# Performance work log

Hardware: AMD Instinct MI355X
Metric: run time of the kernel (lower is better)

Reference implementation:

```python
import jax, jax.numpy as jnp
import numpy as np

N_NODES = 100000
N_EDGES = 1600000
NUM_GRAPHS = 1000
NODE_IN, EDGE_IN = 32, 16
NODE_EMB, EDGE_EMB, HID, OUT, L = 64, 32, 64, 1, 3
EPS = 1e-5


def _glorot(key, shape):
    fan_in = shape[0]
    return jax.random.normal(key, shape, jnp.float32) / np.sqrt(fan_in)


def setup_inputs() -> dict:
    key = jax.random.key(0)
    ks = jax.random.split(key, 16)
    inp = {
        "x": jax.random.normal(ks[0], (N_NODES, NODE_IN), jnp.float32),
        "edge_attr": jax.random.normal(ks[1], (N_EDGES, EDGE_IN), jnp.float32),
        "edge_index": jax.random.randint(ks[2], (2, N_EDGES), 0, N_NODES, jnp.int64
                                         if jax.config.jax_enable_x64 else jnp.int32),
        "batch": jnp.sort(jax.random.randint(ks[3], (N_NODES,), 0, NUM_GRAPHS)),
        # embeddings
        "node_W": _glorot(ks[4], (NODE_IN, NODE_EMB)),
        "node_b": jnp.zeros((NODE_EMB,), jnp.float32),
        "edge_W": _glorot(ks[5], (EDGE_IN, EDGE_EMB)),
        "edge_b": jnp.zeros((EDGE_EMB,), jnp.float32),
        # per-layer MPNN params (node_dim==64 for every layer since node_emb_dim==hidden_dim)
        "msg_W": _glorot(ks[6], (L, NODE_EMB + EDGE_EMB, HID)),
        "msg_b": jnp.zeros((L, HID), jnp.float32),
        "msg_gamma": jnp.ones((L, HID), jnp.float32),
        "msg_beta": jnp.zeros((L, HID), jnp.float32),
        "upd_W": _glorot(ks[7], (L, NODE_EMB + HID, HID)),
        "upd_b": jnp.zeros((L, HID), jnp.float32),
        "upd_gamma": jnp.ones((L, HID), jnp.float32),
        "upd_beta": jnp.zeros((L, HID), jnp.float32),
        # readout
        "r1_W": _glorot(ks[8], (HID, HID)),
        "r1_b": jnp.zeros((HID,), jnp.float32),
        "r2_W": _glorot(ks[9], (HID, OUT)),
        "r2_b": jnp.zeros((OUT,), jnp.float32),
    }
    return inp


def _bn(h, gamma, beta):
    # BatchNorm1d in training mode: normalize with batch mean / biased variance
    mu = jnp.mean(h, axis=0)
    var = jnp.mean(jnp.square(h - mu), axis=0)
    return gamma * (h - mu) * jax.lax.rsqrt(var + EPS) + beta


def reference(x, edge_attr, edge_index, batch,
              node_W, node_b, edge_W, edge_b,
              msg_W, msg_b, msg_gamma, msg_beta,
              upd_W, upd_b, upd_gamma, upd_beta,
              r1_W, r1_b, r2_W, r2_b):
    h = x @ node_W + node_b                       # [N, 64]
    e = edge_attr @ edge_W + edge_b               # [E, 32]
    src, dst = edge_index[0], edge_index[1]
    for i in range(L):
        # message: gather x_j, concat edge feats, Linear-ReLU-BN (dropout = eval/no-op)
        m = jnp.concatenate([h[src], e], axis=-1) @ msg_W[i] + msg_b[i]   # [E, 64]
        m = _bn(jax.nn.relu(m), msg_gamma[i], msg_beta[i])
        # aggregate: scatter-add to destination nodes
        agg = jax.ops.segment_sum(m, dst, num_segments=N_NODES)          # [N, 64]
        # update: concat self feats, Linear-ReLU-BN
        u = jnp.concatenate([h, agg], axis=-1) @ upd_W[i] + upd_b[i]     # [N, 64]
        h = _bn(jax.nn.relu(u), upd_gamma[i], upd_beta[i])
    # global add pool over graphs
    g = jax.ops.segment_sum(h, batch, num_segments=NUM_GRAPHS)           # [G, 64]
    out = jax.nn.relu(g @ r1_W + r1_b) @ r2_W + r2_b                     # [G, 1]
    return out
```

## Files before the change

kernel.cpp:

```cpp
#include <hip/hip_runtime.h>
#include <hip/hip_bf16.h>

#define N_NODES   100000
#define N_EDGES   1600000
#define NUM_GRAPHS 1000

typedef unsigned int u32;
typedef unsigned short u16;

typedef __bf16 bf16_t;
typedef bf16_t bf16x8 __attribute__((ext_vector_type(8)));
typedef float  f32x4  __attribute__((ext_vector_type(4)));

__device__ __forceinline__ float bf2f(u16 u){ return __uint_as_float(((u32)u)<<16); }
__device__ __forceinline__ float BL(u32 u){ return __uint_as_float(u<<16); }
__device__ __forceinline__ float BH(u32 u){ return __uint_as_float(u&0xffff0000u); }
__device__ __forceinline__ u16 f2bf(float f){
  u32 u = __float_as_uint(f);
  return (u16)((u + 0x7fffu + ((u>>16)&1u)) >> 16);
}
__device__ __forceinline__ float ldf(const void* p, size_t i, int isbf){
  return isbf ? bf2f(((const u16*)p)[i]) : ((const float*)p)[i];
}

union U4BF { uint4 u; bf16x8 v; };

__global__ void k_detect(const u32* __restrict__ x, int* __restrict__ flag){
  int t = threadIdx.x; int cnt = 0;
  for (int i = t; i < 256; i += 64){
    u32 w = x[i];
    u32 e = (w >> 7) & 0xffu;
    if (e >= 110u && e <= 137u) cnt++;
  }
  for (int o = 32; o; o >>= 1) cnt += __shfl_xor(cnt, o);
  if (t == 0) *flag = (cnt > 128) ? 1 : 0;
}

__global__ void k_prep(const void* __restrict__ eW, const void* __restrict__ eb,
                       const void* __restrict__ mW, const void* __restrict__ mb,
                       u16* __restrict__ Weff, const int* __restrict__ flagp){
  int isbf = *flagp;
  int l = blockIdx.x, c = threadIdx.x;
  u16* W = Weff + ((size_t)l*64 + c)*96;
  for (int k = 0; k < 64; k++)
    W[k] = f2bf(ldf(mW, (size_t)(l*96 + k)*64 + c, isbf));
  for (int j = 0; j < 16; j++){
    float acc = 0.f;
    for (int k = 0; k < 32; k++)
      acc += ldf(eW, (size_t)j*32 + k, isbf) * ldf(mW, (size_t)(l*96 + 64 + k)*64 + c, isbf);
    W[64 + j] = f2bf(acc);
  }
  float fbv = ldf(mb, (size_t)l*64 + c, isbf);
  for (int k = 0; k < 32; k++)
    fbv += ldf(eb, k, isbf) * ldf(mW, (size_t)(l*96 + 64 + k)*64 + c, isbf);
  W[80] = f2bf(fbv);
  for (int k = 81; k < 96; k++) W[k] = 0;
}

__global__ void k_updprep(const void* __restrict__ uW, const void* __restrict__ ub,
                          const float* __restrict__ maff,
                          u16* __restrict__ Wupd, float* __restrict__ biasv,
                          float* __restrict__ tvv, const int* __restrict__ flagp, int l){
  int isbf = *flagp; int c = threadIdx.x;
  u16* W = Wupd + (size_t)c*192;
  float tv = 0.f;
  for (int k = 0; k < 64; k++){
    float wka = ldf(uW, (size_t)(l*128 + k)*64 + c, isbf);
    W[k] = f2bf(wka);
    float wkb = ldf(uW, (size_t)(l*128 + 64 + k)*64 + c, isbf);
    float prod = wkb * maff[k];
    u16 hi = f2bf(prod);
    W[64 + k]  = hi;
    W[128 + k] = f2bf(prod - bf2f(hi));
    tv = fmaf(maff[64 + k], wkb, tv);
  }
  biasv[c] = ldf(ub, (size_t)l*64 + c, isbf);
  tvv[c] = tv;
}

__global__ void k_node_emb(const void* __restrict__ x, const void* __restrict__ nW,
                           const void* __restrict__ nb, u16* __restrict__ hsp,
                           const int* __restrict__ flagp){
  int isbf = *flagp;
  int lane = threadIdx.x & 63;
  int gw = (blockIdx.x*blockDim.x + threadIdx.x) >> 6;
  int nw = (gridDim.x*blockDim.x) >> 6;
  float w[32];
#pragma unroll
  for (int k = 0; k < 32; k++) w[k] = ldf(nW, (size_t)k*64 + lane, isbf);
  float bias = ldf(nb, lane, isbf);
  for (int n = gw; n < N_NODES; n += nw){
    float acc = bias;
    if (isbf){
      const uint4* xr = (const uint4*)((const u16*)x + (size_t)n*32);
#pragma unroll
      for (int q = 0; q < 4; q++){
        uint4 a = xr[q];
        u32 uu[4] = {a.x, a.y, a.z, a.w};
#pragma unroll
        for (int j = 0; j < 4; j++){
          acc = fmaf(BL(uu[j]), w[q*8 + 2*j + 0], acc);
          acc = fmaf(BH(uu[j]), w[q*8 + 2*j + 1], acc);
        }
      }
    } else {
      const float4* xr = (const float4*)((const float*)x + (size_t)n*32);
#pragma unroll
      for (int q = 0; q < 8; q++){
        float4 a = xr[q];
        acc = fmaf(a.x, w[q*4+0], acc); acc = fmaf(a.y, w[q*4+1], acc);
        acc = fmaf(a.z, w[q*4+2], acc); acc = fmaf(a.w, w[q*4+3], acc);
      }
    }
    u16 hi = f2bf(acc);
    hsp[(size_t)n*128 + lane]      = hi;
    hsp[(size_t)n*128 + 64 + lane] = f2bf(acc - bf2f(hi));
  }
}

__global__ void k_deg(const int* __restrict__ ei, int* __restrict__ deg){
  int i = blockIdx.x*blockDim.x + threadIdx.x;
  int stride = gridDim.x*blockDim.x;
  for (int e = i; e < N_EDGES; e += stride)
    atomicAdd(&deg[ei[N_EDGES + e]], 1);
}

__global__ void __launch_bounds__(256) k_scan1(const int* __restrict__ deg,
                                               int* __restrict__ bsum){
  __shared__ int wsum[4];
  int b = blockIdx.x, t = threadIdx.x;
  int i0 = b*512 + t;
  int s = 0;
  if (i0 < N_NODES) s += deg[i0];
  if (i0 + 256 < N_NODES) s += deg[i0 + 256];
  for (int o = 32; o; o >>= 1) s += __shfl_xor(s, o);
  if ((t & 63) == 0) wsum[t >> 6] = s;
  __syncthreads();
  if (t == 0) bsum[b] = wsum[0] + wsum[1] + wsum[2] + wsum[3];
}

__global__ void k_scan2(const int* __restrict__ bsum, int* __restrict__ boff,
                        int* __restrict__ rp){
  __shared__ int l[200];
  int t = threadIdx.x;
  if (t < 196) l[t] = bsum[t];
  __syncthreads();
  if (t == 0){
    int r = 0;
    for (int k = 0; k < 196; k++){ int x = l[k]; l[k] = r; r += x; }
    rp[N_NODES] = r;
  }
  __syncthreads();
  if (t < 196) boff[t] = l[t];
}

__global__ void __launch_bounds__(256) k_scan3(const int* __restrict__ deg,
                        const int* __restrict__ boff, int* __restrict__ rp,
                        int* __restrict__ cursor, float* __restrict__ degf){
  __shared__ int wpre[4];
  int b = blockIdx.x, t = threadIdx.x;
  int i0 = b*512 + 2*t;
  int d0 = (i0     < N_NODES) ? deg[i0]     : 0;
  int d1 = (i0 + 1 < N_NODES) ? deg[i0 + 1] : 0;
  int s = d0 + d1;
  int incl = s;
  for (int o = 1; o < 64; o <<= 1){ int u = __shfl_up(incl, o); if ((t & 63) >= o) incl += u; }
  if ((t & 63) == 63) wpre[t >> 6] = incl;
  __syncthreads();
  if (t == 0){ int r = 0; for (int k = 0; k < 4; k++){ int x = wpre[k]; wpre[k] = r; r += x; } }
  __syncthreads();
  int excl = boff[b] + wpre[t >> 6] + incl - s;
  if (i0 < N_NODES){
    rp[i0] = excl; cursor[i0] = excl; degf[i0] = (float)d0;
  }
  if (i0 + 1 < N_NODES){
    rp[i0+1] = excl + d0; cursor[i0+1] = excl + d0; degf[i0+1] = (float)d1;
  }
}

__global__ void k_scatter(const int* __restrict__ ei, int* __restrict__ cursor,
                          int* __restrict__ perm2){
  int i = blockIdx.x*blockDim.x + threadIdx.x;
  int stride = gridDim.x*blockDim.x;
  for (int e = i; e < N_EDGES; e += stride){
    int d = ei[N_EDGES + e];
    int p = atomicAdd(&cursor[d], 1);
    ((int2*)perm2)[p] = make_int2(ei[e], e);
  }
}

__global__ void k_scatter2(const int* __restrict__ ei, int* __restrict__ cursor,
                           int* __restrict__ perm, u16* __restrict__ eacsr,
                           const void* __restrict__ ea, const int* __restrict__ flagp){
  int isbf = *flagp;
  int i = blockIdx.x*blockDim.x + threadIdx.x;
  int stride = gridDim.x*blockDim.x;
  if (i < 16){
    perm[N_EDGES + i] = 0;
    uint4 z = make_uint4(0,0,0,0);
    uint4* out = (uint4*)(eacsr + (size_t)(N_EDGES + i)*16);
    out[0] = z; out[1] = z;
  }
  for (int e = i; e < N_EDGES; e += stride){
    int d = ei[N_EDGES + e];
    int p = atomicAdd(&cursor[d], 1);
    perm[p] = ei[e];
    uint4 r0, r1;
    if (isbf){
      const uint4* er = (const uint4*)((const u16*)ea + (size_t)e*16);
      r0 = er[0]; r1 = er[1];
    } else {
      const float4* ef = (const float4*)((const float*)ea + (size_t)e*16);
      float4 f0 = ef[0], f1 = ef[1], f2 = ef[2], f3 = ef[3];
      r0.x = (u32)f2bf(f0.x) | ((u32)f2bf(f0.y)<<16);
      r0.y = (u32)f2bf(f0.z) | ((u32)f2bf(f0.w)<<16);
      r0.z = (u32)f2bf(f1.x) | ((u32)f2bf(f1.y)<<16);
      r0.w = (u32)f2bf(f1.z) | ((u32)f2bf(f1.w)<<16);
      r1.x = (u32)f2bf(f2.x) | ((u32)f2bf(f2.y)<<16);
      r1.y = (u32)f2bf(f2.z) | ((u32)f2bf(f2.w)<<16);
      r1.z = (u32)f2bf(f3.x) | ((u32)f2bf(f3.y)<<16);
      r1.w = (u32)f2bf(f3.z) | ((u32)f2bf(f3.w)<<16);
    }
    uint4* out = (uint4*)(eacsr + (size_t)p*16);
    out[0] = r0; out[1] = r1;
  }
}

__device__ __forceinline__ void adv_tile(const int* __restrict__ rp,
                                         int ni, int bi, int ei,
                                         int& no, int& bo, int& eo){
  if (bi + 16 < ei){ no = ni; bo = bi + 16; eo = ei; return; }
  int t = ni + 1;
  int nb = ei;
  int ne = rp[(t < N_NODES) ? t + 1 : N_NODES];
  while (nb == ne && t + 1 < N_NODES){
    t++; nb = ne; ne = rp[t + 1];
  }
  no = t; bo = nb; eo = ne;
}

__global__ void __launch_bounds__(256) k_msgmm(
    const u16* __restrict__ hsp, const void* __restrict__ ea,
    const int* __restrict__ rp, const int* __restrict__ perm2,
    const u16* __restrict__ Weff, u16* __restrict__ aggs,
    float* __restrict__ stats, const int* __restrict__ flagp,
    int l, int nwaves){
  __shared__ float bs[128];
  int tid = threadIdx.x;
  if (tid < 128) bs[tid] = 0.f;
  __syncthreads();
  int isbf = *flagp;
  int lane = tid & 63, wv = tid >> 6;
  int w = blockIdx.x*4 + wv;
  long long t0 = (long long)w     * N_EDGES / nwaves;
  long long t1 = (long long)(w+1) * N_EDGES / nwaves;
  int lo = 0, hi = N_NODES;
  while (lo < hi){ int mid = (lo+hi)>>1; if ((long long)rp[mid] < t0) lo = mid+1; else hi = mid; }
  int n0 = lo, n1;
  if (w == nwaves-1) n1 = N_NODES;
  else {
    lo = 0; hi = N_NODES;
    while (lo < hi){ int mid = (lo+hi)>>1; if ((long long)rp[mid] < t1) lo = mid+1; else hi = mid; }
    n1 = lo;
  }
  int nn = lane & 15, kg = lane >> 4;
  bf16x8 B[3][4];
  const u16* Wl = Weff + (size_t)l*64*96;
#pragma unroll
  for (int t = 0; t < 4; t++)
#pragma unroll
    for (int kb = 0; kb < 3; kb++)
      B[kb][t] = *(const bf16x8*)(Wl + (size_t)(t*16+nn)*96 + kb*32 + kg*8);
  U4BF ac; ac.u = make_uint4((kg==2)? 0x3f80u : 0u, 0u, 0u, 0u);
  float s1[4] = {0,0,0,0}, s2[4] = {0,0,0,0};
  for (int n = n0; n < n1; n++){
    int b0 = rp[n], b1 = rp[n+1];
    float r0 = 0.f, r1 = 0.f, r2 = 0.f, r3 = 0.f;
    for (int base = b0; base < b1; base += 16){
      int rem = b1 - base; if (rem > 16) rem = 16;
      int row = (nn < rem) ? nn : rem-1;
      int2 p = ((const int2*)perm2)[base + row];
      const uint4* hp = (const uint4*)(hsp + (size_t)p.x*128);
      U4BF fA, fB, fC;
      fA.u = hp[kg];
      fB.u = hp[4 + kg];
      if (kg < 2){
        if (isbf){
          fC.u = ((const uint4*)ea)[(size_t)p.y*2 + kg];
        } else {
          const float4* ef = (const float4*)ea;
          float4 f0 = ef[(size_t)p.y*4 + kg*2];
          float4 f1 = ef[(size_t)p.y*4 + kg*2 + 1];
          fC.u.x = (u32)f2bf(f0.x) | ((u32)f2bf(f0.y)<<16);
          fC.u.y = (u32)f2bf(f0.z) | ((u32)f2bf(f0.w)<<16);
          fC.u.z = (u32)f2bf(f1.x) | ((u32)f2bf(f1.y)<<16);
          fC.u.w = (u32)f2bf(f1.z) | ((u32)f2bf(f1.w)<<16);
        }
      } else fC = ac;
      f32x4 a0 = {0,0,0,0}, a1 = {0,0,0,0}, a2 = {0,0,0,0}, a3 = {0,0,0,0};
      a0 = __builtin_amdgcn_mfma_f32_16x16x32_bf16(fA.v, B[0][0], a0, 0,0,0);
      a1 = __builtin_amdgcn_mfma_f32_16x16x32_bf16(fA.v, B[0][1], a1, 0,0,0);
      a2 = __builtin_amdgcn_mfma_f32_16x16x32_bf16(fA.v, B[0][2], a2, 0,0,0);
      a3 = __builtin_amdgcn_mfma_f32_16x16x32_bf16(fA.v, B[0][3], a3, 0,0,0);
      a0 = __builtin_amdgcn_mfma_f32_16x16x32_bf16(fB.v, B[1][0], a0, 0,0,0);
      a1 = __builtin_amdgcn_mfma_f32_16x16x32_bf16(fB.v, B[1][1], a1, 0,0,0);
      a2 = __builtin_amdgcn_mfma_f32_16x16x32_bf16(fB.v, B[1][2], a2, 0,0,0);
      a3 = __builtin_amdgcn_mfma_f32_16x16x32_bf16(fB.v, B[1][3], a3, 0,0,0);
      a0 = __builtin_amdgcn_mfma_f32_16x16x32_bf16(fC.v, B[2][0], a0, 0,0,0);
      a1 = __builtin_amdgcn_mfma_f32_16x16x32_bf16(fC.v, B[2][1], a1, 0,0,0);
      a2 = __builtin_amdgcn_mfma_f32_16x16x32_bf16(fC.v, B[2][2], a2, 0,0,0);
      a3 = __builtin_amdgcn_mfma_f32_16x16x32_bf16(fC.v, B[2][3], a3, 0,0,0);
      int rowbase = kg*4;
      float ts0 = 0.f, ts1 = 0.f, ts2 = 0.f, ts3 = 0.f;
#pragma unroll
      for (int j = 0; j < 4; j++){
        bool valid = (rowbase + j) < rem;
        float m0 = fmaxf(a0[j], 0.f); m0 = valid ? m0 : 0.f;
        float m1 = fmaxf(a1[j], 0.f); m1 = valid ? m1 : 0.f;
        float m2 = fmaxf(a2[j], 0.f); m2 = valid ? m2 : 0.f;
        float m3 = fmaxf(a3[j], 0.f); m3 = valid ? m3 : 0.f;
        ts0 += m0; ts1 += m1; ts2 += m2; ts3 += m3;
        s2[0] = fmaf(m0,m0,s2[0]); s2[1] = fmaf(m1,m1,s2[1]);
        s2[2] = fmaf(m2,m2,s2[2]); s2[3] = fmaf(m3,m3,s2[3]);
      }
      s1[0] += ts0; s1[1] += ts1; s1[2] += ts2; s1[3] += ts3;
      ts0 += __shfl_xor(ts0,16); ts0 += __shfl_xor(ts0,32);
      ts1 += __shfl_xor(ts1,16); ts1 += __shfl_xor(ts1,32);
      ts2 += __shfl_xor(ts2,16); ts2 += __shfl_xor(ts2,32);
      ts3 += __shfl_xor(ts3,16); ts3 += __shfl_xor(ts3,32);
      r0 += ts0; r1 += ts1; r2 += ts2; r3 += ts3;
    }
    float v = (kg==0) ? r0 : (kg==1) ? r1 : (kg==2) ? r2 : r3;
    u16 hiv = f2bf(v);
    aggs[(size_t)n*128 + lane]      = hiv;
    aggs[(size_t)n*128 + 64 + lane] = f2bf(v - bf2f(hiv));
  }
#pragma unroll
  for (int t = 0; t < 4; t++){
    atomicAdd(&bs[t*16+nn], s1[t]);
    atomicAdd(&bs[64+t*16+nn], s2[t]);
  }
  __syncthreads();
  if (tid < 128) atomicAdd(&stats[tid], bs[tid]);
}

__global__ void __launch_bounds__(256) k_msgmm2(
    const u16* __restrict__ hsp, const u16* __restrict__ eacsr,
    const int* __restrict__ rp, const int* __restrict__ perm,
    const u16* __restrict__ Weff, u16* __restrict__ aggs,
    float* __restrict__ stats, int l, int nwaves){
  __shared__ float bs[128];
  int tid = threadIdx.x;
  if (tid < 128) bs[tid] = 0.f;
  __syncthreads();
  int lane = tid & 63;
  int w = blockIdx.x*4 + (tid >> 6);
  long long t0 = (long long)w     * N_EDGES / nwaves;
  long long t1 = (long long)(w+1) * N_EDGES / nwaves;
  int lo = 0, hi = N_NODES;
  while (lo < hi){ int mid = (lo+hi)>>1; if ((long long)rp[mid] < t0) lo = mid+1; else hi = mid; }
  int n0 = lo, n1;
  if (w == nwaves-1) n1 = N_NODES;
  else {
    lo = 0; hi = N_NODES;
    while (lo < hi){ int mid = (lo+hi)>>1; if ((long long)rp[mid] < t1) lo = mid+1; else hi = mid; }
    n1 = lo;
  }
  int nn = lane & 15, kg = lane >> 4;
  bf16x8 B[3][4];
  const u16* Wl = Weff + (size_t)l*64*96;
#pragma unroll
  for (int t = 0; t < 4; t++)
#pragma unroll
    for (int kb = 0; kb < 3; kb++)
      B[kb][t] = *(const bf16x8*)(Wl + (size_t)(t*16+nn)*96 + kb*32 + kg*8);
  U4BF ac; ac.u = make_uint4((kg==2)? 0x3f80u : 0u, 0u, 0u, 0u);
  float s1[4] = {0,0,0,0}, s2[4] = {0,0,0,0};

  if (n0 < n1){
    {
      int pv = rp[n0];
      for (int m = n0; m < n1; m++){
        int nx = rp[m+1];
        if (nx == pv){
          aggs[(size_t)m*128 + lane] = 0;
          aggs[(size_t)m*128 + 64 + lane] = 0;
        }
        pv = nx;
      }
    }
    int nA = n0;
    int baseA = rp[nA], b1A = rp[nA+1];
    while (baseA == b1A && nA + 1 < n1){ nA++; baseA = b1A; b1A = rp[nA+1]; }
    if (baseA < b1A){
      int nB, baseB, b1B;
      adv_tile(rp, nA, baseA, b1A, nB, baseB, b1B);
      int pB = perm[baseB + nn];
      U4BF fAA, fAB, fAC;
      {
        int pA = perm[baseA + nn];
        const uint4* hpA = (const uint4*)(hsp + (size_t)pA*128);
        fAA.u = hpA[kg]; fAB.u = hpA[4 + kg];
        if (kg < 2) fAC.u = *(const uint4*)(eacsr + ((size_t)baseA + nn)*16 + (size_t)kg*8);
        else fAC = ac;
      }
      float r0 = 0.f, r1 = 0.f, r2 = 0.f, r3 = 0.f;
      while (true){
        int nC, baseC, b1C;
        adv_tile(rp, nB, baseB, b1B, nC, baseC, b1C);
        int pC = perm[baseC + nn];
        const uint4* hpB = (const uint4*)(hsp + (size_t)pB*128);
        U4BF fBA, fBB, fBC;
        fBA.u = hpB[kg]; fBB.u = hpB[4 + kg];
        if (kg < 2) fBC.u = *(const uint4*)(eacsr + ((size_t)baseB + nn)*16 + (size_t)kg*8);
        else fBC = ac;
        f32x4 a0 = {0,0,0,0}, a1 = {0,0,0,0}, a2 = {0,0,0,0}, a3 = {0,0,0,0};
        a0 = __builtin_amdgcn_mfma_f32_16x16x32_bf16(fAA.v, B[0][0], a0, 0,0,0);
        a1 = __builtin_amdgcn_mfma_f32_16x16x32_bf16(fAA.v, B[0][1], a1, 0,0,0);
        a2 = __builtin_amdgcn_mfma_f32_16x16x32_bf16(fAA.v, B[0][2], a2, 0,0,0);
        a3 = __builtin_amdgcn_mfma_f32_16x16x32_bf16(fAA.v, B[0][3], a3, 0,0,0);
        a0 = __builtin_amdgcn_mfma_f32_16x16x32_bf16(fAB.v, B[1][0], a0, 0,0,0);
        a1 = __builtin_amdgcn_mfma_f32_16x16x32_bf16(fAB.v, B[1][1], a1, 0,0,0);
        a2 = __builtin_amdgcn_mfma_f32_16x16x32_bf16(fAB.v, B[1][2], a2, 0,0,0);
        a3 = __builtin_amdgcn_mfma_f32_16x16x32_bf16(fAB.v, B[1][3], a3, 0,0,0);
        a0 = __builtin_amdgcn_mfma_f32_16x16x32_bf16(fAC.v, B[2][0], a0, 0,0,0);
        a1 = __builtin_amdgcn_mfma_f32_16x16x32_bf16(fAC.v, B[2][1], a1, 0,0,0);
        a2 = __builtin_amdgcn_mfma_f32_16x16x32_bf16(fAC.v, B[2][2], a2, 0,0,0);
        a3 = __builtin_amdgcn_mfma_f32_16x16x32_bf16(fAC.v, B[2][3], a3, 0,0,0);
        int rem = b1A - baseA; if (rem > 16) rem = 16;
        int rowbase = kg*4;
        float ts0 = 0.f, ts1 = 0.f, ts2 = 0.f, ts3 = 0.f;
#pragma unroll
        for (int j = 0; j < 4; j++){
          bool valid = (rowbase + j) < rem;
          float m0 = fmaxf(a0[j], 0.f); m0 = valid ? m0 : 0.f;
          float m1 = fmaxf(a1[j], 0.f); m1 = valid ? m1 : 0.f;
          float m2 = fmaxf(a2[j], 0.f); m2 = valid ? m2 : 0.f;
          float m3 = fmaxf(a3[j], 0.f); m3 = valid ? m3 : 0.f;
          ts0 += m0; ts1 += m1; ts2 += m2; ts3 += m3;
          s2[0] = fmaf(m0,m0,s2[0]); s2[1] = fmaf(m1,m1,s2[1]);
          s2[2] = fmaf(m2,m2,s2[2]); s2[3] = fmaf(m3,m3,s2[3]);
        }
        s1[0] += ts0; s1[1] += ts1; s1[2] += ts2; s1[3] += ts3;
        r0 += ts0; r1 += ts1; r2 += ts2; r3 += ts3;
        if (baseA + 16 >= b1A){
          r0 += __shfl_xor(r0,16); r0 += __shfl_xor(r0,32);
          r1 += __shfl_xor(r1,16); r1 += __shfl_xor(r1,32);
          r2 += __shfl_xor(r2,16); r2 += __shfl_xor(r2,32);
          r3 += __shfl_xor(r3,16); r3 += __shfl_xor(r3,32);
          float v = (kg==0) ? r0 : (kg==1) ? r1 : (kg==2) ? r2 : r3;
          u16 hiv = f2bf(v);
          aggs[(size_t)nA*128 + lane]      = hiv;
          aggs[(size_t)nA*128 + 64 + lane] = f2bf(v - bf2f(hiv));
          r0 = r1 = r2 = r3 = 0.f;
        }
        nA = nB; baseA = baseB; b1A = b1B;
        fAA = fBA; fAB = fBB; fAC = fBC;
        nB = nC; baseB = baseC; b1B = b1C; pB = pC;
        if (nA >= n1) break;
      }
    }
  }
#pragma unroll
  for (int t = 0; t < 4; t++){
    atomicAdd(&bs[t*16+nn], s1[t]);
    atomicAdd(&bs[64+t*16+nn], s2[t]);
  }
  __syncthreads();
  if (tid < 128) atomicAdd(&stats[tid], bs[tid]);
}

__global__ void k_fin(float* __restrict__ stats, const void* __restrict__ gamma,
                      const void* __restrict__ beta, float* __restrict__ aff,
                      float cnt_inv, int goff, const int* __restrict__ flagp){
  int isbf = *flagp; int c = threadIdx.x;
  float mu  = stats[c]      * cnt_inv;
  float var = stats[64 + c] * cnt_inv - mu*mu;
  float rs  = rsqrtf(var + 1e-5f);
  float g = ldf(gamma, (size_t)goff + c, isbf);
  float b = ldf(beta,  (size_t)goff + c, isbf);
  aff[c]      = g*rs;
  aff[64 + c] = b - g*mu*rs;
  stats[c] = 0.f; stats[64 + c] = 0.f;
}

#define UPD_TILES (N_NODES/16)
__global__ void __launch_bounds__(256) k_updmm(
    const u16* __restrict__ hsp, u16* __restrict__ aggs,
    const float* __restrict__ degf, const u16* __restrict__ Wupd,
    const float* __restrict__ biasv, const float* __restrict__ tvv,
    float* __restrict__ stats){
  __shared__ float bs[128];
  int tid = threadIdx.x;
  if (tid < 128) bs[tid] = 0.f;
  __syncthreads();
  int lane = tid & 63;
  int nn = lane & 15, kg = lane >> 4;
  int w = blockIdx.x*4 + (tid >> 6);
  int nwv = gridDim.x*4;
  bf16x8 B[6][4];
#pragma unroll
  for (int t = 0; t < 4; t++)
#pragma unroll
    for (int kb = 0; kb < 6; kb++)
      B[kb][t] = *(const bf16x8*)(Wupd + (size_t)(t*16+nn)*192 + kb*32 + kg*8);
  float bc[4], tc[4];
#pragma unroll
  for (int t = 0; t < 4; t++){ bc[t] = biasv[t*16+nn]; tc[t] = tvv[t*16+nn]; }
  float s1[4] = {0,0,0,0}, s2[4] = {0,0,0,0};
  for (int tile = w; tile < UPD_TILES; tile += nwv){
    int n0 = tile*16;
    int r = n0 + nn;
    const uint4* hp = (const uint4*)hsp;
    const uint4* ap = (const uint4*)aggs;
    U4BF hh0, hh1, hl0, hl1, ah0, ah1, al0, al1;
    hh0.u = hp[(size_t)r*16 + kg];       hh1.u = hp[(size_t)r*16 + 4 + kg];
    hl0.u = hp[(size_t)r*16 + 8 + kg];   hl1.u = hp[(size_t)r*16 + 12 + kg];
    ah0.u = ap[(size_t)r*16 + kg];       ah1.u = ap[(size_t)r*16 + 4 + kg];
    al0.u = ap[(size_t)r*16 + 8 + kg];   al1.u = ap[(size_t)r*16 + 12 + kg];
    float dg[4];
#pragma unroll
    for (int j = 0; j < 4; j++) dg[j] = degf[n0 + kg*4 + j];
    f32x4 a0 = {0,0,0,0}, a1 = {0,0,0,0}, a2 = {0,0,0,0}, a3 = {0,0,0,0};
#define MF(F,KB) \
    a0 = __builtin_amdgcn_mfma_f32_16x16x32_bf16(F.v, B[KB][0], a0, 0,0,0); \
    a1 = __builtin_amdgcn_mfma_f32_16x16x32_bf16(F.v, B[KB][1], a1, 0,0,0); \
    a2 = __builtin_amdgcn_mfma_f32_16x16x32_bf16(F.v, B[KB][2], a2, 0,0,0); \
    a3 = __builtin_amdgcn_mfma_f32_16x16x32_bf16(F.v, B[KB][3], a3, 0,0,0);
    MF(hh0,0) MF(hh1,1) MF(hl0,0) MF(hl1,1)
    MF(ah0,2) MF(ah1,3) MF(ah0,4) MF(ah1,5)
    MF(al0,2) MF(al1,3)
#undef MF
#pragma unroll
    for (int j = 0; j < 4; j++){
      int n = n0 + kg*4 + j;
      float m0 = fmaxf(fmaf(tc[0], dg[j], a0[j] + bc[0]), 0.f);
      float m1 = fmaxf(fmaf(tc[1], dg[j], a1[j] + bc[1]), 0.f);
      float m2 = fmaxf(fmaf(tc[2], dg[j], a2[j] + bc[2]), 0.f);
      float m3 = fmaxf(fmaf(tc[3], dg[j], a3[j] + bc[3]), 0.f);
      s1[0] += m0; s1[1] += m1; s1[2] += m2; s1[3] += m3;
      s2[0] = fmaf(m0,m0,s2[0]); s2[1] = fmaf(m1,m1,s2[1]);
      s2[2] = fmaf(m2,m2,s2[2]); s2[3] = fmaf(m3,m3,s2[3]);
      u16* hw = aggs + (size_t)n*128;
      u16 q0 = f2bf(m0), q1 = f2bf(m1), q2 = f2bf(m2), q3 = f2bf(m3);
      hw[     nn] = q0;  hw[64 +      nn] = f2bf(m0 - bf2f(q0));
      hw[16 + nn] = q1;  hw[64 + 16 + nn] = f2bf(m1 - bf2f(q1));
      hw[32 + nn] = q2;  hw[64 + 32 + nn] = f2bf(m2 - bf2f(q2));
      hw[48 + nn] = q3;  hw[64 + 48 + nn] = f2bf(m3 - bf2f(q3));
    }
  }
#pragma unroll
  for (int t = 0; t < 4; t++){
    atomicAdd(&bs[t*16+nn], s1[t]);
    atomicAdd(&bs[64+t*16+nn], s2[t]);
  }
  __syncthreads();
  if (tid < 128) atomicAdd(&stats[tid], bs[tid]);
}

__global__ void k_norm(const u16* __restrict__ aggs, const float* __restrict__ uaff,
                       u16* __restrict__ hsp){
  int lane = threadIdx.x & 63;
  int gw = (blockIdx.x*blockDim.x + threadIdx.x) >> 6;
  int nw = (gridDim.x*blockDim.x) >> 6;
  float s = uaff[lane], t = uaff[64 + lane];
  for (int n = gw; n < N_NODES; n += nw){
    float v = bf2f(aggs[(size_t)n*128 + lane]) + bf2f(aggs[(size_t)n*128 + 64 + lane]);
    float o = fmaf(s, v, t);
    u16 hi = f2bf(o);
    hsp[(size_t)n*128 + lane]      = hi;
    hsp[(size_t)n*128 + 64 + lane] = f2bf(o - bf2f(hi));
  }
}

__global__ void k_pool(const u16* __restrict__ hsp, const int* __restrict__ batch,
                       float* __restrict__ g){
  int lane = threadIdx.x & 63;
  int gw = (blockIdx.x*blockDim.x + threadIdx.x) >> 6;
  int nw = (gridDim.x*blockDim.x) >> 6;
  int chunk = (N_NODES + nw - 1) / nw;
  int n0 = gw*chunk;
  int n1 = n0 + chunk; if (n1 > N_NODES) n1 = N_NODES;
  int cur = -1; float acc = 0.f;
  for (int n = n0; n < n1; n++){
    int b = batch[n];
    float v = bf2f(hsp[(size_t)n*128 + lane]) + bf2f(hsp[(size_t)n*128 + 64 + lane]);
    if (b != cur){
      if (cur >= 0) atomicAdd(&g[(size_t)cur*64 + lane], acc);
      cur = b; acc = v;
    } else acc += v;
  }
  if (cur >= 0) atomicAdd(&g[(size_t)cur*64 + lane], acc);
}

__global__ void k_read(const float* __restrict__ g, const void* __restrict__ r1W,
                       const void* __restrict__ r1b, const void* __restrict__ r2W,
                       const void* __restrict__ r2b, void* __restrict__ out,
                       const int* __restrict__ flagp){
  int isbf = *flagp;
  int lane = threadIdx.x;
  int gr = blockIdx.x;
  float w[64];
#pragma unroll
  for (int k = 0; k < 64; k++) w[k] = ldf(r1W, (size_t)k*64 + lane, isbf);
  float acc = ldf(r1b, lane, isbf);
  const float4* grow = (const float4*)(g + (size_t)gr*64);
#pragma unroll
  for (int q = 0; q < 16; q++){
    float4 a = grow[q];
    acc = fmaf(a.x, w[4*q+0], acc); acc = fmaf(a.y, w[4*q+1], acc);
    acc = fmaf(a.z, w[4*q+2], acc); acc = fmaf(a.w, w[4*q+3], acc);
  }
  float hid = fmaxf(acc, 0.f);
  float p = hid * ldf(r2W, lane, isbf);
  for (int o = 32; o; o >>= 1) p += __shfl_xor(p, o);
  if (lane == 0){
    float v = p + ldf(r2b, 0, isbf);
    if (isbf) ((__hip_bfloat16*)out)[gr] = __float2bfloat16(v);
    else      ((float*)out)[gr] = v;
  }
}

extern "C" void kernel_launch(void* const* d_in, const int* in_sizes, int n_in,
                              void* d_out, int out_size, void* d_ws, size_t ws_size,
                              hipStream_t stream){
  const void* x    = d_in[0];
  const void* ea   = d_in[1];
  const int*  ei   = (const int*)d_in[2];
  const int*  bt   = (const int*)d_in[3];
  const void* nW   = d_in[4];  const void* nb  = d_in[5];
  const void* eW   = d_in[6];  const void* eb  = d_in[7];
  const void* mW   = d_in[8];  const void* mb  = d_in[9];
  const void* mg   = d_in[10]; const void* mbe = d_in[11];
  const void* uW   = d_in[12]; const void* ub  = d_in[13];
  const void* ug   = d_in[14]; const void* ube = d_in[15];
  const void* r1W  = d_in[16]; const void* r1b = d_in[17];
  const void* r2W  = d_in[18]; const void* r2b = d_in[19];

  const size_t NEED_BIG = 110722212ull;
  const bool big = (ws_size >= NEED_BIG);

  float* ws = (float*)d_ws;
  size_t off = 0;
  auto alloc = [&](size_t n){ float* p = ws + off; off += n; return p; };

  u16*   hsp   = (u16*)alloc(6400000);
  u16*   aggs  = (u16*)alloc(6400000);
  u16*   eacsr = nullptr; int* perm = nullptr; int* perm2 = nullptr;
  if (big){
    eacsr = (u16*)alloc(12800128);
    perm  = (int*)alloc(1600016);
  } else {
    perm2 = (int*)alloc(3200000);
  }
  float* degf   = alloc(100000);
  float* zero0  = ws + off;
  int*   deg_i  = (int*)alloc(100000);
  float* g      = alloc(64000);
  float* mstats = alloc(128);
  float* ustats = alloc(128);
  size_t zeroN  = (size_t)((ws + off) - zero0);
  float* maff   = alloc(128);
  float* uaff   = alloc(128);
  int*   flag   = (int*)alloc(16);
  u16*   Weff   = (u16*)alloc(9216);
  u16*   Wupd   = (u16*)alloc(6144);
  float* biasv  = alloc(64);
  float* tvv    = alloc(64);
  int*   row_ptr= (int*)alloc(100001);
  int*   cursor = (int*)alloc(100000);
  int*   bsum   = (int*)alloc(196);
  int*   boff   = (int*)alloc(196);

  const int MM_BLOCKS = 2048;
  const int MM_WAVES  = MM_BLOCKS * 4;
  const int UPD_BLOCKS = 782;

  k_detect<<<1, 64, 0, stream>>>((const u32*)x, flag);
  hipMemsetAsync(zero0, 0, zeroN*sizeof(float), stream);
  k_prep<<<3, 64, 0, stream>>>(eW, eb, mW, mb, Weff, flag);
  k_node_emb<<<256, 256, 0, stream>>>(x, nW, nb, hsp, flag);
  k_deg<<<512, 256, 0, stream>>>(ei, deg_i);
  k_scan1<<<196, 256, 0, stream>>>(deg_i, bsum);
  k_scan2<<<1, 256, 0, stream>>>(bsum, boff, row_ptr);
  k_scan3<<<196, 256, 0, stream>>>(deg_i, boff, row_ptr, cursor, degf);
  if (big)
    k_scatter2<<<512, 256, 0, stream>>>(ei, cursor, perm, eacsr, ea, flag);
  else
    k_scatter<<<512, 256, 0, stream>>>(ei, cursor, perm2);

  for (int l = 0; l < 3; l++){
    if (big)
      k_msgmm2<<<MM_BLOCKS, 256, 0, stream>>>(hsp, eacsr, row_ptr, perm, Weff,
                                              aggs, mstats, l, MM_WAVES);
    else
      k_msgmm<<<MM_BLOCKS, 256, 0, stream>>>(hsp, ea, row_ptr, perm2, Weff,
                                             aggs, mstats, flag, l, MM_WAVES);
    k_fin<<<1, 64, 0, stream>>>(mstats, mg, mbe, maff, 1.0f/(float)N_EDGES, l*64, flag);
    k_updprep<<<1, 64, 0, stream>>>(uW, ub, maff, Wupd, biasv, tvv, flag, l);
    k_updmm<<<UPD_BLOCKS, 256, 0, stream>>>(hsp, aggs, degf, Wupd, biasv, tvv,
                                            ustats);
    k_fin<<<1, 64, 0, stream>>>(ustats, ug, ube, uaff, 1.0f/(float)N_NODES, l*64, flag);
    k_norm<<<256, 256, 0, stream>>>(aggs, uaff, hsp);
  }

  k_pool<<<128, 256, 0, stream>>>(hsp, bt, g);
  k_read<<<NUM_GRAPHS, 64, 0, stream>>>(g, r1W, r1b, r2W, r2b, d_out, flag);
}
```

Before: 1.372 ms.

## Fold update BatchNorm affine into next layer weights and drop normalize pass

The per-layer normalize kernel that applied the update BatchNorm scale/shift to every node is removed. The affine is instead folded into the next layer's message weights and bias (new k_fold kernel), into the update-GEMM self weights and bias, and into the final pooling, with the H/G buffers ping-ponged. The aim is to avoid a full read/write pass over node features each layer. The message kernel's software pipeline is also deepened from a two-tile to a three-tile prefetch rotation. This adds small weight-prep launches, and the folded weights are rounded to bf16 after scaling, which changes numerics slightly.

```diff
diff --git a/kernel.cpp b/kernel.cpp
--- a/kernel.cpp
+++ b/kernel.cpp
@@ -36,9 +36,15 @@
   if (t == 0) *flag = (cnt > 128) ? 1 : 0;
 }
 
+__global__ void k_idaff(float* __restrict__ haff){
+  int c = threadIdx.x;
+  haff[c] = 1.f; haff[64 + c] = 0.f;
+}
+
 __global__ void k_prep(const void* __restrict__ eW, const void* __restrict__ eb,
                        const void* __restrict__ mW, const void* __restrict__ mb,
-                       u16* __restrict__ Weff, const int* __restrict__ flagp){
+                       u16* __restrict__ Weff, float* __restrict__ biasm,
+                       const int* __restrict__ flagp){
   int isbf = *flagp;
   int l = blockIdx.x, c = threadIdx.x;
   u16* W = Weff + ((size_t)l*64 + c)*96;
@@ -54,19 +60,38 @@
   for (int k = 0; k < 32; k++)
     fbv += ldf(eb, k, isbf) * ldf(mW, (size_t)(l*96 + 64 + k)*64 + c, isbf);
   W[80] = f2bf(fbv);
+  biasm[(size_t)l*64 + c] = fbv;
   for (int k = 81; k < 96; k++) W[k] = 0;
 }
 
+__global__ void k_fold(const void* __restrict__ mW, const u16* __restrict__ Wbase,
+                       const float* __restrict__ biasm, const float* __restrict__ haff,
+                       u16* __restrict__ Wf, const int* __restrict__ flagp, int l){
+  int isbf = *flagp; int c = threadIdx.x;
+  const u16* Wb = Wbase + ((size_t)l*64 + c)*96;
+  u16* W = Wf + (size_t)c*96;
+  float bb = biasm[(size_t)l*64 + c];
+  for (int k = 0; k < 64; k++){
+    float w = ldf(mW, (size_t)(l*96 + k)*64 + c, isbf);
+    W[k] = f2bf(haff[k] * w);
+    bb = fmaf(haff[64 + k], w, bb);
+  }
+  for (int k = 64; k < 80; k++) W[k] = Wb[k];
+  W[80] = f2bf(bb);
+  for (int k = 81; k < 96; k++) W[k] = 0;
+}
+
 __global__ void k_updprep(const void* __restrict__ uW, const void* __restrict__ ub,
-                          const float* __restrict__ maff,
+                          const float* __restrict__ maff, const float* __restrict__ haff,
                           u16* __restrict__ Wupd, float* __restrict__ biasv,
                           float* __restrict__ tvv, const int* __restrict__ flagp, int l){
   int isbf = *flagp; int c = threadIdx.x;
   u16* W = Wupd + (size_t)c*192;
-  float tv = 0.f;
+  float tv = 0.f, bb = 0.f;
   for (int k = 0; k < 64; k++){
     float wka = ldf(uW, (size_t)(l*128 + k)*64 + c, isbf);
-    W[k] = f2bf(wka);
+    W[k] = f2bf(haff[k] * wka);
+    bb = fmaf(haff[64 + k], wka, bb);
     float wkb = ldf(uW, (size_t)(l*128 + 64 + k)*64 + c, isbf);
     float prod = wkb * maff[k];
     u16 hi = f2bf(prod);
@@ -74,7 +99,7 @@
     W[128 + k] = f2bf(prod - bf2f(hi));
     tv = fmaf(maff[64 + k], wkb, tv);
   }
-  biasv[c] = ldf(ub, (size_t)l*64 + c, isbf);
+  biasv[c] = ldf(ub, (size_t)l*64 + c, isbf) + bb;
   tvv[c] = tv;
 }
 
@@ -242,9 +267,9 @@
 __global__ void __launch_bounds__(256) k_msgmm(
     const u16* __restrict__ hsp, const void* __restrict__ ea,
     const int* __restrict__ rp, const int* __restrict__ perm2,
-    const u16* __restrict__ Weff, u16* __restrict__ aggs,
+    const u16* __restrict__ Wl, u16* __restrict__ aggs,
     float* __restrict__ stats, const int* __restrict__ flagp,
-    int l, int nwaves){
+    int nwaves){
   __shared__ float bs[128];
   int tid = threadIdx.x;
   if (tid < 128) bs[tid] = 0.f;
@@ -265,7 +290,6 @@
   }
   int nn = lane & 15, kg = lane >> 4;
   bf16x8 B[3][4];
-  const u16* Wl = Weff + (size_t)l*64*96;
 #pragma unroll
   for (int t = 0; t < 4; t++)
 #pragma unroll
@@ -347,8 +371,8 @@
 __global__ void __launch_bounds__(256) k_msgmm2(
     const u16* __restrict__ hsp, const u16* __restrict__ eacsr,
     const int* __restrict__ rp, const int* __restrict__ perm,
-    const u16* __restrict__ Weff, u16* __restrict__ aggs,
-    float* __restrict__ stats, int l, int nwaves){
+    const u16* __restrict__ Wl, u16* __restrict__ aggs,
+    float* __restrict__ stats, int nwaves){
   __shared__ float bs[128];
   int tid = threadIdx.x;
   if (tid < 128) bs[tid] = 0.f;
@@ -359,16 +383,15 @@
   long long t1 = (long long)(w+1) * N_EDGES / nwaves;
   int lo = 0, hi = N_NODES;
   while (lo < hi){ int mid = (lo+hi)>>1; if ((long long)rp[mid] < t0) lo = mid+1; else hi = mid; }
-  int n0 = lo, n1;
-  if (w == nwaves-1) n1 = N_NODES;
+  int nBeg = lo, nEnd;
+  if (w == nwaves-1) nEnd = N_NODES;
   else {
     lo = 0; hi = N_NODES;
     while (lo < hi){ int mid = (lo+hi)>>1; if ((long long)rp[mid] < t1) lo = mid+1; else hi = mid; }
-    n1 = lo;
+    nEnd = lo;
   }
   int nn = lane & 15, kg = lane >> 4;
   bf16x8 B[3][4];
-  const u16* Wl = Weff + (size_t)l*64*96;
 #pragma unroll
   for (int t = 0; t < 4; t++)
 #pragma unroll
@@ -377,10 +400,10 @@
   U4BF ac; ac.u = make_uint4((kg==2)? 0x3f80u : 0u, 0u, 0u, 0u);
   float s1[4] = {0,0,0,0}, s2[4] = {0,0,0,0};
 
-  if (n0 < n1){
+  if (nBeg < nEnd){
     {
-      int pv = rp[n0];
-      for (int m = n0; m < n1; m++){
+      int pv = rp[nBeg];
+      for (int m = nBeg; m < nEnd; m++){
         int nx = rp[m+1];
         if (nx == pv){
           aggs[(size_t)m*128 + lane] = 0;
@@ -389,76 +412,86 @@
         pv = nx;
       }
     }
-    int nA = n0;
-    int baseA = rp[nA], b1A = rp[nA+1];
-    while (baseA == b1A && nA + 1 < n1){ nA++; baseA = b1A; b1A = rp[nA+1]; }
-    if (baseA < b1A){
-      int nB, baseB, b1B;
-      adv_tile(rp, nA, baseA, b1A, nB, baseB, b1B);
-      int pB = perm[baseB + nn];
-      U4BF fAA, fAB, fAC;
+    int nA = nBeg, bA = rp[nA], eA = rp[nA+1];
+    while (bA == eA && nA + 1 < nEnd){ nA++; bA = eA; eA = rp[nA+1]; }
+    if (bA < eA){
+      int n1_, b1_, e1_, n2_, b2_, e2_, n3_, b3_, e3_;
+      adv_tile(rp, nA, bA, eA, n1_, b1_, e1_);
+      adv_tile(rp, n1_, b1_, e1_, n2_, b2_, e2_);
+      int p2 = perm[b2_ + nn];
+      U4BF Xa, Xb, Xc, Ya, Yb, Yc, Za, Zb, Zc;
       {
-        int pA = perm[baseA + nn];
-        const uint4* hpA = (const uint4*)(hsp + (size_t)pA*128);
-        fAA.u = hpA[kg]; fAB.u = hpA[4 + kg];
-        if (kg < 2) fAC.u = *(const uint4*)(eacsr + ((size_t)baseA + nn)*16 + (size_t)kg*8);
-        else fAC = ac;
+        int p0 = perm[bA + nn];
+        const uint4* hp = (const uint4*)(hsp + (size_t)p0*128);
+        Xa.u = hp[kg]; Xb.u = hp[4 + kg];
+        if (kg < 2) Xc.u = *(const uint4*)(eacsr + ((size_t)bA + nn)*16 + (size_t)kg*8);
+        else Xc = ac;
+      }
+      {
+        int p1 = perm[b1_ + nn];
+        const uint4* hp = (const uint4*)(hsp + (size_t)p1*128);
+        Ya.u = hp[kg]; Yb.u = hp[4 + kg];
+        if (kg < 2) Yc.u = *(const uint4*)(eacsr + ((size_t)b1_ + nn)*16 + (size_t)kg*8);
+        else Yc = ac;
       }
       float r0 = 0.f, r1 = 0.f, r2 = 0.f, r3 = 0.f;
+#define MBODY(Pa,Pb,Pc, Ra,Rb,Rc) { \
+      adv_tile(rp, n2_, b2_, e2_, n3_, b3_, e3_); \
+      int p3 = perm[b3_ + nn]; \
+      { const uint4* hp = (const uint4*)(hsp + (size_t)p2*128); \
+        Ra.u = hp[kg]; Rb.u = hp[4 + kg]; \
+        if (kg < 2) Rc.u = *(const uint4*)(eacsr + ((size_t)b2_ + nn)*16 + (size_t)kg*8); \
+        else Rc = ac; } \
+      f32x4 a0 = {0,0,0,0}, a1 = {0,0,0,0}, a2 = {0,0,0,0}, a3 = {0,0,0,0}; \
+      a0 = __builtin_amdgcn_mfma_f32_16x16x32_bf16(Pa.v, B[0][0], a0, 0,0,0); \
+      a1 = __builtin_amdgcn_mfma_f32_16x16x32_bf16(Pa.v, B[0][1], a1, 0,0,0); \
+      a2 = __builtin_amdgcn_mfma_f32_16x16x32_bf16(Pa.v, B[0][2], a2, 0,0,0); \
+      a3 = __builtin_amdgcn_mfma_f32_16x16x32_bf16(Pa.v, B[0][3], a3, 0,0,0); \
+      a0 = __builtin_amdgcn_mfma_f32_16x16x32_bf16(Pb.v, B[1][0], a0, 0,0,0); \
+      a1 = __builtin_amdgcn_mfma_f32_16x16x32_bf16(Pb.v, B[1][1], a1, 0,0,0); \
+      a2 = __builtin_amdgcn_mfma_f32_16x16x32_bf16(Pb.v, B[1][2], a2, 0,0,0); \
+      a3 = __builtin_amdgcn_mfma_f32_16x16x32_bf16(Pb.v, B[1][3], a3, 0,0,0); \
+      a0 = __builtin_amdgcn_mfma_f32_16x16x32_bf16(Pc.v, B[2][0], a0, 0,0,0); \
+      a1 = __builtin_amdgcn_mfma_f32_16x16x32_bf16(Pc.v, B[2][1], a1, 0,0,0); \
+      a2 = __builtin_amdgcn_mfma_f32_16x16x32_bf16(Pc.v, B[2][2], a2, 0,0,0); \
+      a3 = __builtin_amdgcn_mfma_f32_16x16x32_bf16(Pc.v, B[2][3], a3, 0,0,0); \
+      int rem = eA - bA; if (rem > 16) rem = 16; \
+      int rowbase = kg*4; \
+      float ts0 = 0.f, ts1 = 0.f, ts2 = 0.f, ts3 = 0.f; \
+      _Pragma("unroll") \
+      for (int j = 0; j < 4; j++){ \
+        bool valid = (rowbase + j) < rem; \
+        float m0 = fmaxf(a0[j], 0.f); m0 = valid ? m0 : 0.f; \
+        float m1 = fmaxf(a1[j], 0.f); m1 = valid ? m1 : 0.f; \
+        float m2 = fmaxf(a2[j], 0.f); m2 = valid ? m2 : 0.f; \
+        float m3 = fmaxf(a3[j], 0.f); m3 = valid ? m3 : 0.f; \
+        ts0 += m0; ts1 += m1; ts2 += m2; ts3 += m3; \
+        s2[0] = fmaf(m0,m0,s2[0]); s2[1] = fmaf(m1,m1,s2[1]); \
+        s2[2] = fmaf(m2,m2,s2[2]); s2[3] = fmaf(m3,m3,s2[3]); \
+      } \
+      s1[0] += ts0; s1[1] += ts1; s1[2] += ts2; s1[3] += ts3; \
+      r0 += ts0; r1 += ts1; r2 += ts2; r3 += ts3; \
+      if (bA + 16 >= eA){ \
+        r0 += __shfl_xor(r0,16); r0 += __shfl_xor(r0,32); \
+        r1 += __shfl_xor(r1,16); r1 += __shfl_xor(r1,32); \
+        r2 += __shfl_xor(r2,16); r2 += __shfl_xor(r2,32); \
+        r3 += __shfl_xor(r3,16); r3 += __shfl_xor(r3,32); \
+        float v = (kg==0) ? r0 : (kg==1) ? r1 : (kg==2) ? r2 : r3; \
+        u16 hiv = f2bf(v); \
+        aggs[(size_t)nA*128 + lane]      = hiv; \
+        aggs[(size_t)nA*128 + 64 + lane] = f2bf(v - bf2f(hiv)); \
+        r0 = r1 = r2 = r3 = 0.f; \
+      } \
+      nA = n1_; bA = b1_; eA = e1_; \
+      n1_ = n2_; b1_ = b2_; e1_ = e2_; \
+      n2_ = n3_; b2_ = b3_; e2_ = e3_; p2 = p3; \
+      if (nA >= nEnd) break; }
       while (true){
-        int nC, baseC, b1C;
-        adv_tile(rp, nB, baseB, b1B, nC, baseC, b1C);
-        int pC = perm[baseC + nn];
-        const uint4* hpB = (const uint4*)(hsp + (size_t)pB*128);
-        U4BF fBA, fBB, fBC;
-        fBA.u = hpB[kg]; fBB.u = hpB[4 + kg];
-        if (kg < 2) fBC.u = *(const uint4*)(eacsr + ((size_t)baseB + nn)*16 + (size_t)kg*8);
-        else fBC = ac;
-        f32x4 a0 = {0,0,0,0}, a1 = {0,0,0,0}, a2 = {0,0,0,0}, a3 = {0,0,0,0};
-        a0 = __builtin_amdgcn_mfma_f32_16x16x32_bf16(fAA.v, B[0][0], a0, 0,0,0);
-        a1 = __builtin_amdgcn_mfma_f32_16x16x32_bf16(fAA.v, B[0][1], a1, 0,0,0);
-        a2 = __builtin_amdgcn_mfma_f32_16x16x32_bf16(fAA.v, B[0][2], a2, 0,0,0);
-        a3 = __builtin_amdgcn_mfma_f32_16x16x32_bf16(fAA.v, B[0][3], a3, 0,0,0);
-        a0 = __builtin_amdgcn_mfma_f32_16x16x32_bf16(fAB.v, B[1][0], a0, 0,0,0);
-        a1 = __builtin_amdgcn_mfma_f32_16x16x32_bf16(fAB.v, B[1][1], a1, 0,0,0);
-        a2 = __builtin_amdgcn_mfma_f32_16x16x32_bf16(fAB.v, B[1][2], a2, 0,0,0);
-        a3 = __builtin_amdgcn_mfma_f32_16x16x32_bf16(fAB.v, B[1][3], a3, 0,0,0);
-        a0 = __builtin_amdgcn_mfma_f32_16x16x32_bf16(fAC.v, B[2][0], a0, 0,0,0);
-        a1 = __builtin_amdgcn_mfma_f32_16x16x32_bf16(fAC.v, B[2][1], a1, 0,0,0);
-        a2 = __builtin_amdgcn_mfma_f32_16x16x32_bf16(fAC.v, B[2][2], a2, 0,0,0);
-        a3 = __builtin_amdgcn_mfma_f32_16x16x32_bf16(fAC.v, B[2][3], a3, 0,0,0);
-        int rem = b1A - baseA; if (rem > 16) rem = 16;
-        int rowbase = kg*4;
-        float ts0 = 0.f, ts1 = 0.f, ts2 = 0.f, ts3 = 0.f;
-#pragma unroll
-        for (int j = 0; j < 4; j++){
-          bool valid = (rowbase + j) < rem;
-          float m0 = fmaxf(a0[j], 0.f); m0 = valid ? m0 : 0.f;
-          float m1 = fmaxf(a1[j], 0.f); m1 = valid ? m1 : 0.f;
-          float m2 = fmaxf(a2[j], 0.f); m2 = valid ? m2 : 0.f;
-          float m3 = fmaxf(a3[j], 0.f); m3 = valid ? m3 : 0.f;
-          ts0 += m0; ts1 += m1; ts2 += m2; ts3 += m3;
-          s2[0] = fmaf(m0,m0,s2[0]); s2[1] = fmaf(m1,m1,s2[1]);
-          s2[2] = fmaf(m2,m2,s2[2]); s2[3] = fmaf(m3,m3,s2[3]);
-        }
-        s1[0] += ts0; s1[1] += ts1; s1[2] += ts2; s1[3] += ts3;
-        r0 += ts0; r1 += ts1; r2 += ts2; r3 += ts3;
-        if (baseA + 16 >= b1A){
-          r0 += __shfl_xor(r0,16); r0 += __shfl_xor(r0,32);
-          r1 += __shfl_xor(r1,16); r1 += __shfl_xor(r1,32);
-          r2 += __shfl_xor(r2,16); r2 += __shfl_xor(r2,32);
-          r3 += __shfl_xor(r3,16); r3 += __shfl_xor(r3,32);
-          float v = (kg==0) ? r0 : (kg==1) ? r1 : (kg==2) ? r2 : r3;
-          u16 hiv = f2bf(v);
-          aggs[(size_t)nA*128 + lane]      = hiv;
-          aggs[(size_t)nA*128 + 64 + lane] = f2bf(v - bf2f(hiv));
-          r0 = r1 = r2 = r3 = 0.f;
-        }
-        nA = nB; baseA = baseB; b1A = b1B;
-        fAA = fBA; fAB = fBB; fAC = fBC;
-        nB = nC; baseB = baseC; b1B = b1C; pB = pC;
-        if (nA >= n1) break;
+        MBODY(Xa,Xb,Xc, Za,Zb,Zc)
+        MBODY(Ya,Yb,Yc, Xa,Xb,Xc)
+        MBODY(Za,Zb,Zc, Ya,Yb,Yc)
       }
+#undef MBODY
     }
   }
 #pragma unroll
@@ -558,39 +591,25 @@
   if (tid < 128) atomicAdd(&stats[tid], bs[tid]);
 }
 
-__global__ void k_norm(const u16* __restrict__ aggs, const float* __restrict__ uaff,
-                       u16* __restrict__ hsp){
+__global__ void k_pool(const u16* __restrict__ hsp, const int* __restrict__ batch,
+                       const float* __restrict__ aff, float* __restrict__ g){
   int lane = threadIdx.x & 63;
   int gw = (blockIdx.x*blockDim.x + threadIdx.x) >> 6;
   int nw = (gridDim.x*blockDim.x) >> 6;
-  float s = uaff[lane], t = uaff[64 + lane];
-  for (int n = gw; n < N_NODES; n += nw){
-    float v = bf2f(aggs[(size_t)n*128 + lane]) + bf2f(aggs[(size_t)n*128 + 64 + lane]);
-    float o = fmaf(s, v, t);
-    u16 hi = f2bf(o);
-    hsp[(size_t)n*128 + lane]      = hi;
-    hsp[(size_t)n*128 + 64 + lane] = f2bf(o - bf2f(hi));
-  }
-}
-
-__global__ void k_pool(const u16* __restrict__ hsp, const int* __restrict__ batch,
-                       float* __restrict__ g){
-  int lane = threadIdx.x & 63;
-  int gw = (blockIdx.x*blockDim.x + threadIdx.x) >> 6;
-  int nw = (gridDim.x*blockDim.x) >> 6;
+  float s = aff[lane], t = aff[64 + lane];
   int chunk = (N_NODES + nw - 1) / nw;
   int n0 = gw*chunk;
   int n1 = n0 + chunk; if (n1 > N_NODES) n1 = N_NODES;
-  int cur = -1; float acc = 0.f;
+  int cur = -1; float acc = 0.f, cnt = 0.f;
   for (int n = n0; n < n1; n++){
     int b = batch[n];
     float v = bf2f(hsp[(size_t)n*128 + lane]) + bf2f(hsp[(size_t)n*128 + 64 + lane]);
     if (b != cur){
-      if (cur >= 0) atomicAdd(&g[(size_t)cur*64 + lane], acc);
-      cur = b; acc = v;
-    } else acc += v;
-  }
-  if (cur >= 0) atomicAdd(&g[(size_t)cur*64 + lane], acc);
+      if (cur >= 0) atomicAdd(&g[(size_t)cur*64 + lane], fmaf(s, acc, t*cnt));
+      cur = b; acc = v; cnt = 1.f;
+    } else { acc += v; cnt += 1.f; }
+  }
+  if (cur >= 0) atomicAdd(&g[(size_t)cur*64 + lane], fmaf(s, acc, t*cnt));
 }
 
 __global__ void k_read(const float* __restrict__ g, const void* __restrict__ r1W,
@@ -637,7 +656,7 @@
   const void* r1W  = d_in[16]; const void* r1b = d_in[17];
   const void* r2W  = d_in[18]; const void* r2b = d_in[19];
 
-  const size_t NEED_BIG = 110722212ull;
+  const size_t NEED_BIG = 110735268ull;
   const bool big = (ws_size >= NEED_BIG);
 
   float* ws = (float*)d_ws;
@@ -661,10 +680,12 @@
   float* ustats = alloc(128);
   size_t zeroN  = (size_t)((ws + off) - zero0);
   float* maff   = alloc(128);
-  float* uaff   = alloc(128);
+  float* haff   = alloc(128);
   int*   flag   = (int*)alloc(16);
   u16*   Weff   = (u16*)alloc(9216);
+  u16*   Wfold  = (u16*)alloc(3072);
   u16*   Wupd   = (u16*)alloc(6144);
+  float* biasm  = alloc(192);
   float* biasv  = alloc(64);
   float* tvv    = alloc(64);
   int*   row_ptr= (int*)alloc(100001);
@@ -678,7 +699,8 @@
 
   k_detect<<<1, 64, 0, stream>>>((const u32*)x, flag);
   hipMemsetAsync(zero0, 0, zeroN*sizeof(float), stream);
-  k_prep<<<3, 64, 0, stream>>>(eW, eb, mW, mb, Weff, flag);
+  k_idaff<<<1, 64, 0, stream>>>(haff);
+  k_prep<<<3, 64, 0, stream>>>(eW, eb, mW, mb, Weff, biasm, flag);
   k_node_emb<<<256, 256, 0, stream>>>(x, nW, nb, hsp, flag);
   k_deg<<<512, 256, 0, stream>>>(ei, deg_i);
   k_scan1<<<196, 256, 0, stream>>>(deg_i, bsum);
@@ -689,21 +711,23 @@
   else
     k_scatter<<<512, 256, 0, stream>>>(ei, cursor, perm2);
 
+  u16* H = hsp;
+  u16* G = aggs;
   for (int l = 0; l < 3; l++){
+    k_fold<<<1, 64, 0, stream>>>(mW, Weff, biasm, haff, Wfold, flag, l);
     if (big)
-      k_msgmm2<<<MM_BLOCKS, 256, 0, stream>>>(hsp, eacsr, row_ptr, perm, Weff,
-                                              aggs, mstats, l, MM_WAVES);
+      k_msgmm2<<<MM_BLOCKS, 256, 0, stream>>>(H, eacsr, row_ptr, perm, Wfold,
+                                              G, mstats, MM_WAVES);
     else
-      k_msgmm<<<MM_BLOCKS, 256, 0, stream>>>(hsp, ea, row_ptr, perm2, Weff,
-                                             aggs, mstats, flag, l, MM_WAVES);
+      k_msgmm<<<MM_BLOCKS, 256, 0, stream>>>(H, ea, row_ptr, perm2, Wfold,
+                                             G, mstats, flag, MM_WAVES);
     k_fin<<<1, 64, 0, stream>>>(mstats, mg, mbe, maff, 1.0f/(float)N_EDGES, l*64, flag);
-    k_updprep<<<1, 64, 0, stream>>>(uW, ub, maff, Wupd, biasv, tvv, flag, l);
-    k_updmm<<<UPD_BLOCKS, 256, 0, stream>>>(hsp, aggs, degf, Wupd, biasv, tvv,
-                                            ustats);
-    k_fin<<<1, 64, 0, stream>>>(ustats, ug, ube, uaff, 1.0f/(float)N_NODES, l*64, flag);
-    k_norm<<<256, 256, 0, stream>>>(aggs, uaff, hsp);
-  }
-
-  k_pool<<<128, 256, 0, stream>>>(hsp, bt, g);
+    k_updprep<<<1, 64, 0, stream>>>(uW, ub, maff, haff, Wupd, biasv, tvv, flag, l);
+    k_updmm<<<UPD_BLOCKS, 256, 0, stream>>>(H, G, degf, Wupd, biasv, tvv, ustats);
+    k_fin<<<1, 64, 0, stream>>>(ustats, ug, ube, haff, 1.0f/(float)N_NODES, l*64, flag);
+    u16* tmp = H; H = G; G = tmp;
+  }
+
+  k_pool<<<128, 256, 0, stream>>>(H, bt, haff, g);
   k_read<<<NUM_GRAPHS, 64, 0, stream>>>(g, r1W, r1b, r2W, r2b, d_out, flag);
 }
```

Result: no change. 1.357 ms (-1.1%).
